# Optimization experiments

Hardware: AMD Instinct MI355X
Metric: run time of the kernel (lower is better)

The kernel has to match this reference:

```python
import jax, jax.numpy as jnp
import numpy as np

C = 512
NUM_HEADS = 8
GROUPS = min(32, C // 4)
EPS = 1e-5
SCALE = (C // NUM_HEADS) ** (-0.5)


def setup_inputs() -> dict:
    key = jax.random.key(0)
    ks = jax.random.split(key, 7)
    B, H, W = 8, 32, 32
    x = jax.random.normal(ks[0], (B, C, H, W), dtype=jnp.float32)
    gamma = jnp.ones((C,), dtype=jnp.float32)
    beta = jnp.zeros((C,), dtype=jnp.float32)
    # 1x1 convs == per-pixel matmuls; store weights as [out, in]
    w_qkv = jax.random.normal(ks[1], (3 * C, C), dtype=jnp.float32) * (C ** -0.5)
    b_qkv = jax.random.normal(ks[2], (3 * C,), dtype=jnp.float32) * 0.01
    w_proj = jax.random.normal(ks[3], (C, C), dtype=jnp.float32) * (C ** -0.5)
    b_proj = jax.random.normal(ks[4], (C,), dtype=jnp.float32) * 0.01
    return {"x": x, "gamma": gamma, "beta": beta, "w_qkv": w_qkv,
            "b_qkv": b_qkv, "w_proj": w_proj, "b_proj": b_proj}


def _group_norm(x, gamma, beta):
    B, Cc, H, W = x.shape
    xg = x.reshape(B, GROUPS, Cc // GROUPS, H, W)
    mean = jnp.mean(xg, axis=(2, 3, 4), keepdims=True)
    var = jnp.var(xg, axis=(2, 3, 4), keepdims=True)
    xg = (xg - mean) * jax.lax.rsqrt(var + EPS)
    x = xg.reshape(B, Cc, H, W)
    return x * gamma[None, :, None, None] + beta[None, :, None, None]


def reference(x, gamma, beta, w_qkv, b_qkv, w_proj, b_proj):
    B, Cc, H, W = x.shape
    nh, hd = NUM_HEADS, Cc // NUM_HEADS
    HW = H * W
    h = _group_norm(x, gamma, beta)
    # 1x1 conv: [B,C,H,W] -> [B,3C,H,W]
    qkv = jnp.einsum('oc,bchw->bohw', w_qkv, h) + b_qkv[None, :, None, None]
    qkv = qkv.reshape(B, 3, nh, hd, HW)
    q, k, v = qkv[:, 0], qkv[:, 1], qkv[:, 2]  # each [B, nh, hd, HW]
    scores = jnp.einsum('bhcq,bhck->bhqk', q, k) * SCALE  # [B, nh, HW, HW]
    attn = jax.nn.softmax(scores, axis=-1)
    out = jnp.einsum('bhqk,bhck->bhcq', attn, v)  # [B, nh, hd, HW]
    out = out.reshape(B, Cc, H, W)
    out = jnp.einsum('oc,bchw->bohw', w_proj, out) + b_proj[None, :, None, None]
    return x + out
```

## Files before the change

### kernel.cpp

```cpp
#include <hip/hip_runtime.h>
#include <stdint.h>
#include <math.h>

#define CDIM 512
#define NHEAD 8
#define HD 64
#define HWD 1024
#define BATCH 8
#define NGRP 32
#define CPG 16
#define EPSV 1e-5f
#define QSCALE 0.125f

typedef __bf16 bf16x8 __attribute__((ext_vector_type(8)));
typedef float f32x4 __attribute__((ext_vector_type(4)));

static __device__ __forceinline__ unsigned short f2bf(float x){
  union { float f; unsigned u; } v; v.f = x;
  unsigned r = v.u + 0x7fffu + ((v.u >> 16) & 1u);
  return (unsigned short)(r >> 16);
}

static __device__ __forceinline__ void gload_lds16(const void* g, void* l){
  __builtin_amdgcn_global_load_lds(
      (const __attribute__((address_space(1))) unsigned int*)g,
      (__attribute__((address_space(3))) unsigned int*)l, 16, 0, 0);
}

__global__ void cvt2_kernel(const float* __restrict__ a, const float* __restrict__ b,
                            unsigned short* __restrict__ oa, unsigned short* __restrict__ ob,
                            int na, int nb){
  int i = (blockIdx.x * blockDim.x + threadIdx.x) * 4;
  const float* src; unsigned short* dst; int j;
  if (i < na){ src = a; dst = oa; j = i; }
  else { j = i - na; if (j >= nb) return; src = b; dst = ob; }
  float4 v = *(const float4*)(src + j);
  ushort4 o;
  o.x = f2bf(v.x); o.y = f2bf(v.y); o.z = f2bf(v.z); o.w = f2bf(v.w);
  *(ushort4*)(dst + j) = o;
}

__global__ __launch_bounds__(256) void gn_kernel(const float* __restrict__ x,
    const float* __restrict__ gamma, const float* __restrict__ beta,
    unsigned short* __restrict__ hT){
  int b   = blockIdx.x >> 5;
  int grp = blockIdx.x & 31;
  int c0  = grp * CPG;
  int t   = threadIdx.x;
  const float* xp = x + ((size_t)b * CDIM + c0) * HWD;
  float vals[CPG][4];
  float s = 0.f, s2 = 0.f;
  #pragma unroll
  for (int j = 0; j < CPG; ++j){
    #pragma unroll
    for (int k = 0; k < 4; ++k){
      float v = xp[j * HWD + t + 256 * k];
      vals[j][k] = v; s += v; s2 += v * v;
    }
  }
  #pragma unroll
  for (int off = 32; off > 0; off >>= 1){
    s  += __shfl_down(s, off);
    s2 += __shfl_down(s2, off);
  }
  __shared__ float red[8];
  __shared__ float stats[2];
  int lane = t & 63, wid = t >> 6;
  if (lane == 0){ red[wid] = s; red[wid + 4] = s2; }
  __syncthreads();
  if (t == 0){
    float ts  = red[0] + red[1] + red[2] + red[3];
    float ts2 = red[4] + red[5] + red[6] + red[7];
    float mean = ts * (1.f / (CPG * HWD));
    float var  = ts2 * (1.f / (CPG * HWD)) - mean * mean;
    stats[0] = mean; stats[1] = rsqrtf(var + EPSV);
  }
  __syncthreads();
  float mean = stats[0], inv = stats[1];
  float gm[CPG], bt[CPG];
  #pragma unroll
  for (int j = 0; j < CPG; ++j){ gm[j] = gamma[c0 + j] * inv; bt[j] = beta[c0 + j]; }
  #pragma unroll
  for (int k = 0; k < 4; ++k){
    unsigned pk[8];
    #pragma unroll
    for (int j = 0; j < 8; ++j){
      unsigned short lo = f2bf((vals[2*j][k]   - mean) * gm[2*j]   + bt[2*j]);
      unsigned short hi = f2bf((vals[2*j+1][k] - mean) * gm[2*j+1] + bt[2*j+1]);
      pk[j] = (unsigned)lo | ((unsigned)hi << 16);
    }
    size_t base = ((size_t)b * HWD + t + 256 * k) * CDIM + c0;
    uint4 a0 = {pk[0], pk[1], pk[2], pk[3]};
    uint4 a1 = {pk[4], pk[5], pk[6], pk[7]};
    *(uint4*)(hT + base)     = a0;
    *(uint4*)(hT + base + 8) = a1;
  }
}

template<int MODE>
__global__ __launch_bounds__(256) void gemm_bt(
    const unsigned short* __restrict__ A,
    const unsigned short* __restrict__ BT,
    const float* __restrict__ bias,
    const float* __restrict__ xres,
    float* __restrict__ outf,
    unsigned short* __restrict__ qT,
    unsigned short* __restrict__ kT,
    unsigned short* __restrict__ vb,
    int M, int N, int K)
{
  __shared__ unsigned short As[128*64];
  __shared__ unsigned short Bs[128*64];
  int n0 = blockIdx.x * 128;
  int m0 = blockIdx.y * 128;
  int b  = blockIdx.z;
  int t  = threadIdx.x;
  int lane = t & 63, wid = t >> 6;
  int wr = wid >> 1, wc = wid & 1;
  int lr = lane & 15, g = lane >> 4;
  const unsigned short* Bb = BT + (size_t)b * N * K;

  int srow = wid * 32 + (lane >> 3);
  int sseg = (lane & 7) ^ (lane >> 3);
  const unsigned short* ag = A  + (size_t)(m0 + srow) * K + sseg * 8;
  const unsigned short* bg = Bb + (size_t)(n0 + srow) * K + sseg * 8;

  f32x4 acc[4][4];
  f32x4 zz = {0.f, 0.f, 0.f, 0.f};
  #pragma unroll
  for (int m = 0; m < 4; ++m)
    #pragma unroll
    for (int n = 0; n < 4; ++n) acc[m][n] = zz;

  for (int k0 = 0; k0 < K; k0 += 64){
    #pragma unroll
    for (int j = 0; j < 4; ++j){
      gload_lds16(ag + (size_t)j*8*K + k0, &As[(wid*32 + j*8)*64]);
      gload_lds16(bg + (size_t)j*8*K + k0, &Bs[(wid*32 + j*8)*64]);
    }
    __syncthreads();
    #pragma unroll
    for (int kk = 0; kk < 2; ++kk){
      unsigned segx = (unsigned)(((kk*4 + g) ^ (lr & 7)) << 4);
      bf16x8 af[4], bfr[4];
      #pragma unroll
      for (int m = 0; m < 4; ++m)
        af[m] = *(const bf16x8*)((const char*)As + (unsigned)((wr*64 + m*16 + lr)*128) + segx);
      #pragma unroll
      for (int n = 0; n < 4; ++n)
        bfr[n] = *(const bf16x8*)((const char*)Bs + (unsigned)((wc*64 + n*16 + lr)*128) + segx);
      #pragma unroll
      for (int m = 0; m < 4; ++m)
        #pragma unroll
        for (int n = 0; n < 4; ++n)
          acc[m][n] = __builtin_amdgcn_mfma_f32_16x16x32_bf16(af[m], bfr[n], acc[m][n], 0, 0, 0);
    }
    __syncthreads();
  }

  if (MODE == 0){
    #pragma unroll
    for (int m = 0; m < 4; ++m){
      int o_base = m0 + wr*64 + m*16 + g*4;
      int s = o_base >> 9;
      int h = (o_base >> 6) & 7;
      int dbase = o_base & 63;
      float bv[4];
      #pragma unroll
      for (int r = 0; r < 4; ++r) bv[r] = bias[o_base + r];
      #pragma unroll
      for (int n = 0; n < 4; ++n){
        int hw = n0 + wc*64 + n*16 + lr;
        if (s == 2){
          int a = hw & 31;
          int hwp = (hw & ~31) | (((a >> 2) & 3) * 8 + (a & 3) + (((a >> 4) & 1) << 2));
          #pragma unroll
          for (int r = 0; r < 4; ++r){
            float val = acc[m][n][r] + bv[r];
            vb[(((size_t)b*NHEAD + h)*HD + dbase + r)*HWD + hwp] = f2bf(val);
          }
        } else {
          float sc = (s == 0) ? QSCALE : 1.f;
          ushort4 pk;
          pk.x = f2bf((acc[m][n][0] + bv[0]) * sc);
          pk.y = f2bf((acc[m][n][1] + bv[1]) * sc);
          pk.z = f2bf((acc[m][n][2] + bv[2]) * sc);
          pk.w = f2bf((acc[m][n][3] + bv[3]) * sc);
          unsigned short* dst = (s == 0) ? qT : kT;
          *(ushort4*)&dst[(((size_t)b*NHEAD + h)*HWD + hw)*HD + dbase] = pk;
        }
      }
    }
  } else {
    #pragma unroll
    for (int m = 0; m < 4; ++m){
      int o0 = m0 + wr*64 + m*16 + g*4;
      #pragma unroll
      for (int n = 0; n < 4; ++n){
        int hw = n0 + wc*64 + n*16 + lr;
        #pragma unroll
        for (int r = 0; r < 4; ++r){
          int o = o0 + r;
          size_t idx = ((size_t)b * M + o) * N + hw;
          outf[idx] = acc[m][n][r] + bias[o] + xres[idx];
        }
      }
    }
  }
}

__global__ __launch_bounds__(512, 4) void attn_flash(
    const unsigned short* __restrict__ qT,
    const unsigned short* __restrict__ kT,
    const unsigned short* __restrict__ vperm,
    unsigned short* __restrict__ aoT)
{
  __shared__ char smem[65536];
  int bh = blockIdx.y;
  int b = bh >> 3, h = bh & 7;
  int t = threadIdx.x;
  int lane = t & 63, wid = t >> 6;
  int lr = lane & 15, g = lane >> 4;
  int q0 = (blockIdx.x * 8 + wid) * 16;

  const unsigned short* qp = qT + ((size_t)bh * HWD + q0) * HD;
  const unsigned short* kp = kT + (size_t)bh * HWD * HD;
  const unsigned short* vp = vperm + (size_t)bh * HD * HWD;

  int ksrow = wid * 16 + (lane >> 3);
  int kseg  = (lane & 7) ^ (lane >> 3);
  const unsigned short* kg = kp + (size_t)ksrow * HD + kseg * 8;
  int vrow0 = wid * 8 + (lane >> 4);

  bf16x8 yq[2];
  yq[0] = *(const bf16x8*)&qp[lr*HD + g*8];
  yq[1] = *(const bf16x8*)&qp[lr*HD + 32 + g*8];

  f32x4 accO[4];
  f32x4 zz = {0.f, 0.f, 0.f, 0.f};
  #pragma unroll
  for (int dt = 0; dt < 4; ++dt) accO[dt] = zz;
  float m = -1e30f, l = 0.f;

  {
    char* kb = smem; char* vbf = smem + 16384;
    #pragma unroll
    for (int j = 0; j < 2; ++j){
      gload_lds16(kg + (size_t)j*8*HD, kb + (wid*16 + j*8)*128);
      int vrow = vrow0 + j*4;
      int vseg = (lane & 15) ^ (vrow & 15);
      gload_lds16(vp + (size_t)vrow*HWD + vseg*8, vbf + (wid*8 + j*4)*256);
    }
  }
  __syncthreads();

  unsigned cur = 0;
  for (int kc = 0; kc < 8; ++kc){
    if (kc < 7){
      char* kb = smem + (cur^1u)*32768u; char* vbf = kb + 16384;
      int c1 = kc + 1;
      #pragma unroll
      for (int j = 0; j < 2; ++j){
        gload_lds16(kg + ((size_t)c1*128 + j*8)*HD, kb + (wid*16 + j*8)*128);
        int vrow = vrow0 + j*4;
        int vseg = (lane & 15) ^ (vrow & 15);
        gload_lds16(vp + (size_t)vrow*HWD + c1*128 + vseg*8, vbf + (wid*8 + j*4)*256);
      }
    }

    char* kbuf = smem + cur*32768u;
    char* vbuf = kbuf + 16384;

    f32x4 s[8];
    __builtin_amdgcn_s_setprio(1);
    #pragma unroll
    for (int tt = 0; tt < 8; ++tt){
      unsigned rb = (unsigned)((tt*16 + lr) * 128);
      bf16x8 k0 = *(const bf16x8*)(kbuf + rb + (((g     ) ^ (lr&7)) << 4));
      bf16x8 k1 = *(const bf16x8*)(kbuf + rb + (((4 + g ) ^ (lr&7)) << 4));
      f32x4 z = zz;
      z = __builtin_amdgcn_mfma_f32_16x16x32_bf16(k0, yq[0], z, 0, 0, 0);
      s[tt] = __builtin_amdgcn_mfma_f32_16x16x32_bf16(k1, yq[1], z, 0, 0, 0);
    }
    __builtin_amdgcn_s_setprio(0);

    float cm = -1e30f;
    #pragma unroll
    for (int tt = 0; tt < 8; ++tt)
      #pragma unroll
      for (int r = 0; r < 4; ++r) cm = fmaxf(cm, s[tt][r]);
    cm = fmaxf(cm, __shfl_xor(cm, 16));
    cm = fmaxf(cm, __shfl_xor(cm, 32));

    float mn = fmaxf(m, cm);
    float f  = __expf(m - mn);
    m = mn;

    float ps = 0.f;
    #pragma unroll
    for (int tt = 0; tt < 8; ++tt)
      #pragma unroll
      for (int r = 0; r < 4; ++r){
        float e = __expf(s[tt][r] - mn);
        s[tt][r] = e; ps += e;
      }
    ps += __shfl_xor(ps, 16);
    ps += __shfl_xor(ps, 32);
    l = l * f + ps;

    float fD[4];
    #pragma unroll
    for (int r = 0; r < 4; ++r) fD[r] = __shfl(f, ((lane >> 4) << 2) + r);
    #pragma unroll
    for (int dt = 0; dt < 4; ++dt)
      #pragma unroll
      for (int r = 0; r < 4; ++r) accO[dt][r] *= fD[r];

    __builtin_amdgcn_s_setprio(1);
    #pragma unroll
    for (int mi = 0; mi < 4; ++mi){
      bf16x8 xp;
      #pragma unroll
      for (int j = 0; j < 4; ++j){
        xp[j]     = (__bf16)s[2*mi][j];
        xp[4 + j] = (__bf16)s[2*mi + 1][j];
      }
      #pragma unroll
      for (int dt = 0; dt < 4; ++dt){
        unsigned rb = (unsigned)((dt*16 + lr) * 256) + (unsigned)((((mi*4 + g) ^ lr) & 15) << 4);
        bf16x8 yv = *(const bf16x8*)(vbuf + rb);
        accO[dt] = __builtin_amdgcn_mfma_f32_16x16x32_bf16(xp, yv, accO[dt], 0, 0, 0);
      }
    }
    __builtin_amdgcn_s_setprio(0);

    __syncthreads();
    cur ^= 1u;
  }

  float invl = 1.f / l;
  float ir[4];
  #pragma unroll
  for (int r = 0; r < 4; ++r) ir[r] = __shfl(invl, ((lane >> 4) << 2) + r);
  #pragma unroll
  for (int dt = 0; dt < 4; ++dt)
    #pragma unroll
    for (int r = 0; r < 4; ++r){
      int qi = q0 + ((lane >> 4) << 2) + r;
      aoT[((size_t)b*HWD + qi)*CDIM + h*HD + dt*16 + lr] = f2bf(accO[dt][r] * ir[r]);
    }
}

extern "C" void kernel_launch(void* const* d_in, const int* in_sizes, int n_in,
                              void* d_out, int out_size, void* d_ws, size_t ws_size,
                              hipStream_t stream) {
  const float* x      = (const float*)d_in[0];
  const float* gamma  = (const float*)d_in[1];
  const float* beta   = (const float*)d_in[2];
  const float* w_qkv  = (const float*)d_in[3];
  const float* b_qkv  = (const float*)d_in[4];
  const float* w_proj = (const float*)d_in[5];
  const float* b_proj = (const float*)d_in[6];
  float* out = (float*)d_out;

  char* ws = (char*)d_ws;
  size_t off = 0;
  unsigned short* wqkv_b  = (unsigned short*)(ws + off); off += (size_t)1536*512*2;
  unsigned short* wproj_b = (unsigned short*)(ws + off); off += (size_t)512*512*2;
  unsigned short* hT      = (unsigned short*)(ws + off); off += (size_t)BATCH*HWD*CDIM*2;
  unsigned short* qT      = (unsigned short*)(ws + off); off += (size_t)BATCH*NHEAD*HWD*HD*2;
  unsigned short* kT      = (unsigned short*)(ws + off); off += (size_t)BATCH*NHEAD*HWD*HD*2;
  unsigned short* vb      = (unsigned short*)(ws + off); off += (size_t)BATCH*NHEAD*HWD*HD*2;
  unsigned short* aoT     = hT;

  cvt2_kernel<<<1024, 256, 0, stream>>>(w_qkv, w_proj, wqkv_b, wproj_b, 1536*512, 512*512);

  gn_kernel<<<BATCH*NGRP, 256, 0, stream>>>(x, gamma, beta, hT);

  gemm_bt<0><<<dim3(HWD/128, 1536/128, BATCH), 256, 0, stream>>>(
      wqkv_b, hT, b_qkv, nullptr, nullptr, qT, kT, vb, 1536, HWD, CDIM);

  attn_flash<<<dim3(HWD/128, BATCH*NHEAD), 512, 0, stream>>>(qT, kT, vb, aoT);

  gemm_bt<1><<<dim3(HWD/128, CDIM/128, BATCH), 256, 0, stream>>>(
      wproj_b, aoT, b_proj, x, out, nullptr, nullptr, nullptr, CDIM, HWD, CDIM);
}
```

Before: 88.31 us.

## Process two query tiles per wave in flash attention, halving block size

Each wave now handles 32 queries (two 16-row tiles) instead of 16, so every K and V fragment read from LDS feeds two MFMAs. Blocks shrink from 512 to 256 threads with the same 128-query tile, and each thread loads twice as many K/V chunks into LDS. This cuts LDS read traffic per MFMA but raises register pressure (doubled accumulators and score arrays), and the launch bounds change may lower occupancy.

```diff
diff --git a/kernel.cpp b/kernel.cpp
--- a/kernel.cpp
+++ b/kernel.cpp
@@ -209,7 +209,7 @@
   }
 }
 
-__global__ __launch_bounds__(512, 4) void attn_flash(
+__global__ __launch_bounds__(256, 2) void attn_flash(
     const unsigned short* __restrict__ qT,
     const unsigned short* __restrict__ kT,
     const unsigned short* __restrict__ vperm,
@@ -221,115 +221,130 @@
   int t = threadIdx.x;
   int lane = t & 63, wid = t >> 6;
   int lr = lane & 15, g = lane >> 4;
-  int q0 = (blockIdx.x * 8 + wid) * 16;
+  int q0 = blockIdx.x * 128 + wid * 32;
 
   const unsigned short* qp = qT + ((size_t)bh * HWD + q0) * HD;
   const unsigned short* kp = kT + (size_t)bh * HWD * HD;
   const unsigned short* vp = vperm + (size_t)bh * HD * HWD;
 
-  int ksrow = wid * 16 + (lane >> 3);
-  int kseg  = (lane & 7) ^ (lane >> 3);
-  const unsigned short* kg = kp + (size_t)ksrow * HD + kseg * 8;
-  int vrow0 = wid * 8 + (lane >> 4);
-
-  bf16x8 yq[2];
-  yq[0] = *(const bf16x8*)&qp[lr*HD + g*8];
-  yq[1] = *(const bf16x8*)&qp[lr*HD + 32 + g*8];
-
-  f32x4 accO[4];
+  int krl  = lane >> 3;
+  int kseg = (lane & 7) ^ krl;
+  const unsigned short* kg = kp + (size_t)(wid*32 + krl) * HD + kseg * 8;
+  unsigned kdst = (unsigned)(wid * 32 * 128);
+  int vrl = lane >> 4;
+  unsigned vdst = 16384u + (unsigned)(wid * 16 * 256);
+
+  bf16x8 yq[2][2];
+  #pragma unroll
+  for (int qt = 0; qt < 2; ++qt){
+    yq[qt][0] = *(const bf16x8*)&qp[(qt*16 + lr)*HD + g*8];
+    yq[qt][1] = *(const bf16x8*)&qp[(qt*16 + lr)*HD + 32 + g*8];
+  }
+
+  f32x4 accO[2][4];
   f32x4 zz = {0.f, 0.f, 0.f, 0.f};
   #pragma unroll
-  for (int dt = 0; dt < 4; ++dt) accO[dt] = zz;
-  float m = -1e30f, l = 0.f;
-
-  {
-    char* kb = smem; char* vbf = smem + 16384;
-    #pragma unroll
-    for (int j = 0; j < 2; ++j){
-      gload_lds16(kg + (size_t)j*8*HD, kb + (wid*16 + j*8)*128);
-      int vrow = vrow0 + j*4;
-      int vseg = (lane & 15) ^ (vrow & 15);
-      gload_lds16(vp + (size_t)vrow*HWD + vseg*8, vbf + (wid*8 + j*4)*256);
-    }
+  for (int qt = 0; qt < 2; ++qt)
+    #pragma unroll
+    for (int dt = 0; dt < 4; ++dt) accO[qt][dt] = zz;
+  float mrun[2] = {-1e30f, -1e30f};
+  float lrun[2] = {0.f, 0.f};
+
+  #pragma unroll
+  for (int j = 0; j < 4; ++j){
+    gload_lds16(kg + (size_t)j*8*HD, smem + kdst + j*8*128);
+    int vseg = (lane & 15) ^ (j*4 + vrl);
+    gload_lds16(vp + (size_t)(wid*16 + j*4 + vrl)*HWD + vseg*8,
+                smem + vdst + j*4*256);
   }
   __syncthreads();
 
   unsigned cur = 0;
   for (int kc = 0; kc < 8; ++kc){
     if (kc < 7){
-      char* kb = smem + (cur^1u)*32768u; char* vbf = kb + 16384;
+      char* bufn = smem + (cur^1u)*32768u;
       int c1 = kc + 1;
       #pragma unroll
-      for (int j = 0; j < 2; ++j){
-        gload_lds16(kg + ((size_t)c1*128 + j*8)*HD, kb + (wid*16 + j*8)*128);
-        int vrow = vrow0 + j*4;
-        int vseg = (lane & 15) ^ (vrow & 15);
-        gload_lds16(vp + (size_t)vrow*HWD + c1*128 + vseg*8, vbf + (wid*8 + j*4)*256);
+      for (int j = 0; j < 4; ++j){
+        gload_lds16(kg + ((size_t)c1*128 + j*8)*HD, bufn + kdst + j*8*128);
+        int vseg = (lane & 15) ^ (j*4 + vrl);
+        gload_lds16(vp + (size_t)(wid*16 + j*4 + vrl)*HWD + c1*128 + vseg*8,
+                    bufn + vdst + j*4*256);
       }
     }
 
     char* kbuf = smem + cur*32768u;
     char* vbuf = kbuf + 16384;
 
-    f32x4 s[8];
+    f32x4 s[2][8];
     __builtin_amdgcn_s_setprio(1);
     #pragma unroll
     for (int tt = 0; tt < 8; ++tt){
       unsigned rb = (unsigned)((tt*16 + lr) * 128);
-      bf16x8 k0 = *(const bf16x8*)(kbuf + rb + (((g     ) ^ (lr&7)) << 4));
-      bf16x8 k1 = *(const bf16x8*)(kbuf + rb + (((4 + g ) ^ (lr&7)) << 4));
-      f32x4 z = zz;
-      z = __builtin_amdgcn_mfma_f32_16x16x32_bf16(k0, yq[0], z, 0, 0, 0);
-      s[tt] = __builtin_amdgcn_mfma_f32_16x16x32_bf16(k1, yq[1], z, 0, 0, 0);
+      bf16x8 k0 = *(const bf16x8*)(kbuf + rb + (((g    ) ^ (lr&7)) << 4));
+      bf16x8 k1 = *(const bf16x8*)(kbuf + rb + (((4 + g) ^ (lr&7)) << 4));
+      #pragma unroll
+      for (int qt = 0; qt < 2; ++qt){
+        f32x4 z = zz;
+        z = __builtin_amdgcn_mfma_f32_16x16x32_bf16(k0, yq[qt][0], z, 0, 0, 0);
+        s[qt][tt] = __builtin_amdgcn_mfma_f32_16x16x32_bf16(k1, yq[qt][1], z, 0, 0, 0);
+      }
     }
     __builtin_amdgcn_s_setprio(0);
 
-    float cm = -1e30f;
-    #pragma unroll
-    for (int tt = 0; tt < 8; ++tt)
-      #pragma unroll
-      for (int r = 0; r < 4; ++r) cm = fmaxf(cm, s[tt][r]);
-    cm = fmaxf(cm, __shfl_xor(cm, 16));
-    cm = fmaxf(cm, __shfl_xor(cm, 32));
-
-    float mn = fmaxf(m, cm);
-    float f  = __expf(m - mn);
-    m = mn;
-
-    float ps = 0.f;
-    #pragma unroll
-    for (int tt = 0; tt < 8; ++tt)
-      #pragma unroll
-      for (int r = 0; r < 4; ++r){
-        float e = __expf(s[tt][r] - mn);
-        s[tt][r] = e; ps += e;
-      }
-    ps += __shfl_xor(ps, 16);
-    ps += __shfl_xor(ps, 32);
-    l = l * f + ps;
-
-    float fD[4];
-    #pragma unroll
-    for (int r = 0; r < 4; ++r) fD[r] = __shfl(f, ((lane >> 4) << 2) + r);
-    #pragma unroll
-    for (int dt = 0; dt < 4; ++dt)
-      #pragma unroll
-      for (int r = 0; r < 4; ++r) accO[dt][r] *= fD[r];
+    #pragma unroll
+    for (int qt = 0; qt < 2; ++qt){
+      float cm = -1e30f;
+      #pragma unroll
+      for (int tt = 0; tt < 8; ++tt)
+        #pragma unroll
+        for (int r = 0; r < 4; ++r) cm = fmaxf(cm, s[qt][tt][r]);
+      cm = fmaxf(cm, __shfl_xor(cm, 16));
+      cm = fmaxf(cm, __shfl_xor(cm, 32));
+
+      float mn = fmaxf(mrun[qt], cm);
+      float f  = __expf(mrun[qt] - mn);
+      mrun[qt] = mn;
+
+      float ps = 0.f;
+      #pragma unroll
+      for (int tt = 0; tt < 8; ++tt)
+        #pragma unroll
+        for (int r = 0; r < 4; ++r){
+          float e = __expf(s[qt][tt][r] - mn);
+          s[qt][tt][r] = e; ps += e;
+        }
+      ps += __shfl_xor(ps, 16);
+      ps += __shfl_xor(ps, 32);
+      lrun[qt] = lrun[qt] * f + ps;
+
+      float fD[4];
+      #pragma unroll
+      for (int r = 0; r < 4; ++r) fD[r] = __shfl(f, g*4 + r);
+      #pragma unroll
+      for (int dt = 0; dt < 4; ++dt)
+        #pragma unroll
+        for (int r = 0; r < 4; ++r) accO[qt][dt][r] *= fD[r];
+    }
 
     __builtin_amdgcn_s_setprio(1);
     #pragma unroll
     for (int mi = 0; mi < 4; ++mi){
-      bf16x8 xp;
-      #pragma unroll
-      for (int j = 0; j < 4; ++j){
-        xp[j]     = (__bf16)s[2*mi][j];
-        xp[4 + j] = (__bf16)s[2*mi + 1][j];
-      }
+      bf16x8 xp[2];
+      #pragma unroll
+      for (int qt = 0; qt < 2; ++qt)
+        #pragma unroll
+        for (int j = 0; j < 4; ++j){
+          xp[qt][j]     = (__bf16)s[qt][2*mi][j];
+          xp[qt][4 + j] = (__bf16)s[qt][2*mi + 1][j];
+        }
       #pragma unroll
       for (int dt = 0; dt < 4; ++dt){
         unsigned rb = (unsigned)((dt*16 + lr) * 256) + (unsigned)((((mi*4 + g) ^ lr) & 15) << 4);
         bf16x8 yv = *(const bf16x8*)(vbuf + rb);
-        accO[dt] = __builtin_amdgcn_mfma_f32_16x16x32_bf16(xp, yv, accO[dt], 0, 0, 0);
+        #pragma unroll
+        for (int qt = 0; qt < 2; ++qt)
+          accO[qt][dt] = __builtin_amdgcn_mfma_f32_16x16x32_bf16(xp[qt], yv, accO[qt][dt], 0, 0, 0);
       }
     }
     __builtin_amdgcn_s_setprio(0);
@@ -338,17 +353,20 @@
     cur ^= 1u;
   }
 
-  float invl = 1.f / l;
-  float ir[4];
-  #pragma unroll
-  for (int r = 0; r < 4; ++r) ir[r] = __shfl(invl, ((lane >> 4) << 2) + r);
-  #pragma unroll
-  for (int dt = 0; dt < 4; ++dt)
-    #pragma unroll
-    for (int r = 0; r < 4; ++r){
-      int qi = q0 + ((lane >> 4) << 2) + r;
-      aoT[((size_t)b*HWD + qi)*CDIM + h*HD + dt*16 + lr] = f2bf(accO[dt][r] * ir[r]);
-    }
+  #pragma unroll
+  for (int qt = 0; qt < 2; ++qt){
+    float invl = 1.f / lrun[qt];
+    float ir[4];
+    #pragma unroll
+    for (int r = 0; r < 4; ++r) ir[r] = __shfl(invl, g*4 + r);
+    #pragma unroll
+    for (int dt = 0; dt < 4; ++dt)
+      #pragma unroll
+      for (int r = 0; r < 4; ++r){
+        int qi = q0 + qt*16 + g*4 + r;
+        aoT[((size_t)b*HWD + qi)*CDIM + h*HD + dt*16 + lr] = f2bf(accO[qt][dt][r] * ir[r]);
+      }
+  }
 }
 
 extern "C" void kernel_launch(void* const* d_in, const int* in_sizes, int n_in,
@@ -380,7 +398,7 @@
   gemm_bt<0><<<dim3(HWD/128, 1536/128, BATCH), 256, 0, stream>>>(
       wqkv_b, hT, b_qkv, nullptr, nullptr, qT, kT, vb, 1536, HWD, CDIM);
 
-  attn_flash<<<dim3(HWD/128, BATCH*NHEAD), 512, 0, stream>>>(qT, kT, vb, aoT);
+  attn_flash<<<dim3(HWD/128, BATCH*NHEAD), 256, 0, stream>>>(qT, kT, vb, aoT);
 
   gemm_bt<1><<<dim3(HWD/128, CDIM/128, BATCH), 256, 0, stream>>>(
       wproj_b, aoT, b_proj, x, out, nullptr, nullptr, nullptr, CDIM, HWD, CDIM);
```

New measurement: 87.23 us. No clear change (-1.2%).
